# Optimization experiments

Measured on AMD Instinct MI355X. Metric: run time of the kernel, lower is better.

## Reference

```python
import jax, jax.numpy as jnp
import numpy as np

NUM_LAYERS = 3
N = 4096
DIM = 512
TOPK = 8
BIG = 1.0e9
EPS_COS = 1e-8
EPS_NORM = 1e-12
BN_EPS = 1e-5
LAM_K = 64.0
LAM_Z = 16.0
SIGMA_INTRA = 0.99
ALPHA = np.linspace(1.0, 1.2, NUM_LAYERS)
BETA = np.linspace(0.0, 0.0, NUM_LAYERS)


def setup_inputs() -> dict:
    key = jax.random.key(0)
    ks = jax.random.split(key, 6)
    feats = jax.random.normal(ks[0], (NUM_LAYERS, N, DIM), dtype=jnp.float32)
    labels = jax.random.randint(ks[1], (N,), 0, 64, dtype=jnp.int64)
    fc1_w = jax.random.normal(ks[2], (NUM_LAYERS, DIM, DIM), dtype=jnp.float32) * (1.0 / np.sqrt(DIM))
    fc2_w = jax.random.normal(ks[3], (NUM_LAYERS, DIM, DIM), dtype=jnp.float32) * (1.0 / np.sqrt(DIM))
    bn_gamma = jnp.ones((NUM_LAYERS, DIM), dtype=jnp.float32)
    bn_beta = jnp.zeros((NUM_LAYERS, DIM), dtype=jnp.float32)
    proj_w = jax.random.normal(ks[4], (768, DIM), dtype=jnp.float32) * (1.0 / np.sqrt(DIM))
    return {"feats": feats, "labels": labels, "fc1_w": fc1_w, "fc2_w": fc2_w,
            "bn_gamma": bn_gamma, "bn_beta": bn_beta, "proj_w": proj_w}


def _l2norm(x, axis=-1):
    return x / jnp.maximum(jnp.linalg.norm(x, axis=axis, keepdims=True), EPS_NORM)


def _pairwise_cosine(G):
    Gn = _l2norm(G)
    sim = Gn @ Gn.T
    return jnp.clip(sim, -1.0 + EPS_COS, 1.0 - EPS_COS)


def _knn_mask(sim, base_mask, topk):
    n = sim.shape[0]
    masked = (sim - BIG * jnp.eye(n, dtype=sim.dtype)) * base_mask - (1.0 - base_mask) * BIG
    k = min(topk, max(n - 1, 1))
    idx = jax.lax.top_k(masked, k)[1]  # [N, k]
    st = jnp.zeros_like(sim).at[jnp.arange(n)[:, None], idx].set(1.0)
    return jnp.maximum(st, st.T)


def _build_intra_inter(sim, labels, topk):
    same = (labels[None, :] == labels[:, None]).astype(sim.dtype)
    diff = 1.0 - same
    m_intra = _knn_mask(sim, same, topk)
    m_inter = _knn_mask(sim, diff, topk)
    sim_intra = jnp.maximum(sim * m_intra, 0.0)
    sim_inter = jnp.maximum(sim * m_inter, 0.0)
    return sim_intra, sim_inter


def _normalize_sym(sim_graph, eps=1e-8):
    d = jnp.maximum(sim_graph.sum(axis=1), eps)
    dinv = d ** -0.5
    return dinv[:, None] * sim_graph * dinv[None, :]  # == diag(dinv) @ S @ diag(dinv)


def _diffusion(K, t_diff=1):
    out = K
    for _ in range(max(t_diff - 1, 0)):
        out = out @ K
    return out


def _bn_train(x, gamma, beta):
    m = x.mean(axis=0)
    v = x.var(axis=0)  # biased, as torch BN training
    return (x - m) / jnp.sqrt(v + BN_EPS) * gamma + beta


def _gam(S, G, w1, w2, gamma, beta):
    Z = S @ (G @ w1.T)
    Z = jax.nn.relu(_bn_train(Z, gamma, beta))
    Z = S @ (Z @ w2.T)
    return Z + G


def reference(feats, labels, fc1_w, fc2_w, bn_gamma, bn_beta, proj_w):
    n = feats.shape[1]
    eye = jnp.eye(n, dtype=feats.dtype)
    same = (labels[None, :] == labels[:, None]).astype(feats.dtype)

    K_list, Z_list = [], []
    for i in range(NUM_LAYERS):
        G = feats[i]
        sim = _pairwise_cosine(G)
        sim_intra, sim_inter = _build_intra_inter(sim, labels, TOPK)
        sim_graph = float(ALPHA[i]) * sim_intra + float(BETA[i]) * sim_inter + 1e-6 * eye
        S = _normalize_sym(sim_graph)
        K = _diffusion(S, t_diff=1)
        Z = _gam(S, G, fc1_w[i], fc2_w[i], bn_gamma[i], bn_beta[i])
        K_list.append(K)
        Z_list.append(Z)

    loss_K = jnp.zeros((), dtype=feats.dtype)
    loss_Z = jnp.zeros((), dtype=feats.dtype)
    for i in range(1, NUM_LAYERS):
        K_tgt = jax.lax.stop_gradient(K_list[i])
        loss_K = loss_K + jnp.mean((K_list[i - 1] - K_tgt) ** 2)
        Zp = _l2norm(Z_list[i - 1] @ proj_w.T)
        Zc = _l2norm(Z_list[i] @ proj_w.T)
        loss_Z = loss_Z + jnp.mean((Zp - jax.lax.stop_gradient(Zc)) ** 2)

    K_idea = _diffusion(same * SIGMA_INTRA, t_diff=1)
    loss_idea = jnp.mean((K_list[-1] - K_idea) ** 2)
    return LAM_K * loss_K + LAM_Z * loss_Z + loss_idea
```

## Files before the change

### kernel.cpp

```cpp
#include <hip/hip_runtime.h>
#include <math.h>

#define NROWS 4096
#define DIM   512
#define NCLS  64
#define CAP   128
#define PD    768
#define NL    3

typedef __attribute__((ext_vector_type(8))) short short8v;
typedef __attribute__((ext_vector_type(4))) float f32x4;

__device__ __forceinline__ unsigned short f2bf(float f) {
  unsigned u = __float_as_uint(f);
  unsigned r = (u + 0x7FFF + ((u >> 16) & 1)) >> 16;
  return (unsigned short)r;
}

__device__ __forceinline__ float waveReduce(float v) {
#pragma unroll
  for (int o = 32; o > 0; o >>= 1) v += __shfl_down(v, o);
  return v;
}

__device__ __forceinline__ float blockReduce(float v) {
  __shared__ float sh[4];
  int lane = threadIdx.x & 63, wv = threadIdx.x >> 6;
  v = waveReduce(v);
  if (lane == 0) sh[wv] = v;
  __syncthreads();
  float t = 0.f;
  if (threadIdx.x == 0) {
    int nw = (blockDim.x + 63) >> 6;
    for (int i = 0; i < nw; ++i) t += sh[i];
  }
  return t;
}

__global__ void k_zerof(float* p, int n) {
  for (int i = blockIdx.x * blockDim.x + threadIdx.x; i < n; i += gridDim.x * blockDim.x) p[i] = 0.f;
}

__global__ __launch_bounds__(256) void k_hist(const int* __restrict__ labels, int* __restrict__ chunkCnt) {
  __shared__ int h[NCLS];
  int t = threadIdx.x;
  if (t < NCLS) h[t] = 0;
  __syncthreads();
  atomicAdd(&h[labels[blockIdx.x * 256 + t]], 1);
  __syncthreads();
  if (t < NCLS) chunkCnt[blockIdx.x * NCLS + t] = h[t];
}

__global__ void k_scan(const int* __restrict__ chunkCnt, int* __restrict__ cnt,
                       int* __restrict__ off, int* __restrict__ chunkBase) {
  __shared__ int sc[NCLS];
  int c = threadIdx.x;
  int tot = 0;
  for (int b = 0; b < 16; ++b) tot += chunkCnt[b * NCLS + c];
  cnt[c] = tot;
  sc[c] = tot;
  __syncthreads();
  if (c == 0) {
    int s = 0;
    for (int i = 0; i < NCLS; ++i) { int tv = sc[i]; sc[i] = s; s += tv; }
  }
  __syncthreads();
  int run = sc[c];
  off[c] = run;
  for (int b = 0; b < 16; ++b) { chunkBase[b * NCLS + c] = run; run += chunkCnt[b * NCLS + c]; }
  if (c == 0) off[NCLS] = NROWS;
}

__global__ __launch_bounds__(256) void k_scatter(const int* __restrict__ labels, const int* __restrict__ chunkBase,
                                                 int* __restrict__ perm, int* __restrict__ clsp) {
  __shared__ int lab[256];
  int t = threadIdx.x;
  int r = blockIdx.x * 256 + t;
  int c = labels[r];
  lab[t] = c;
  __syncthreads();
  int rank = 0;
  for (int j = 0; j < t; ++j) rank += (lab[j] == c);
  int pos = chunkBase[blockIdx.x * NCLS + c] + rank;
  perm[pos] = r;
  clsp[pos] = c;
}

__global__ __launch_bounds__(128) void k_prep(const float* __restrict__ feats, const int* __restrict__ perm,
                                              unsigned short* __restrict__ Gpb, float* __restrict__ invn) {
  __shared__ float red[2];
  int l = blockIdx.y;
  const float* G = feats + (size_t)l * NROWS * DIM;
  unsigned short* Gp = Gpb + (size_t)l * NROWS * DIM;
  int row = blockIdx.x, t = threadIdx.x;
  const float4* src = (const float4*)(G + (size_t)perm[row] * DIM);
  float4 v = src[t];
  ushort4 b;
  b.x = f2bf(v.x); b.y = f2bf(v.y); b.z = f2bf(v.z); b.w = f2bf(v.w);
  *(ushort4*)(Gp + (size_t)row * DIM + t * 4) = b;
  float ss = v.x * v.x + v.y * v.y + v.z * v.z + v.w * v.w;
  ss = waveReduce(ss);
  if ((t & 63) == 0) red[t >> 6] = ss;
  __syncthreads();
  if (t == 0) invn[l * NROWS + row] = 1.f / fmaxf(sqrtf(red[0] + red[1]), 1e-12f);
}

__global__ void k_tobf16(const float4* __restrict__ src, ushort4* __restrict__ dst, int n4) {
  int i = blockIdx.x * blockDim.x + threadIdx.x;
  if (i < n4) {
    float4 v = src[i];
    ushort4 o;
    o.x = f2bf(v.x); o.y = f2bf(v.y); o.z = f2bf(v.z); o.w = f2bf(v.w);
    dst[i] = o;
  }
}

__global__ __launch_bounds__(256) void k_sim(const unsigned short* __restrict__ Gpb,
                                             const float* __restrict__ invn,
                                             const int* __restrict__ cnt, const int* __restrict__ off,
                                             float* __restrict__ sim) {
  int l = blockIdx.z;
  const unsigned short* Gp = Gpb + (size_t)l * NROWS * DIM;
  const float* inv = invn + (size_t)l * NROWS;
  float* sm = sim + (size_t)l * NCLS * CAP * CAP;
  int c = blockIdx.y;
  int n = min(cnt[c], CAP);
  int ti = blockIdx.x >> 2, tj = blockIdx.x & 3;
  if (ti * 32 >= n || tj * 32 >= n) return;
  int base = off[c];
  __shared__ short As[32][40];
  __shared__ short Bs[32][40];
  const int t = threadIdx.x;
  const int lane = t & 63, wv = t >> 6;
  const int qi = wv >> 1, qj = wv & 1;
  const int fr = lane & 15, kg = lane >> 4;
  const int half = t >> 7, tt = t & 127;
  const int srow = tt >> 2, scol = (tt & 3) * 8;
  int gr = (half ? tj : ti) * 32 + srow;
  const unsigned short* ps = Gp + (size_t)(base + min(gr, n - 1)) * DIM + scol;
  short* dst = half ? &Bs[srow][scol] : &As[srow][scol];
  f32x4 acc = {};
  for (int k0 = 0; k0 < DIM; k0 += 32) {
    short8v v = *(const short8v*)(ps + k0);
    __syncthreads();
    *(short8v*)dst = v;
    __syncthreads();
    short8v af = *(const short8v*)&As[qi * 16 + fr][kg * 8];
    short8v bf = *(const short8v*)&Bs[qj * 16 + fr][kg * 8];
    acc = __builtin_amdgcn_mfma_f32_16x16x32_bf16(af, bf, acc, 0, 0, 0);
  }
  int gj = tj * 32 + qj * 16 + fr;
  int r0 = ti * 32 + qi * 16 + kg * 4;
  if (gj < n) {
    float sj = inv[base + gj];
#pragma unroll
    for (int r = 0; r < 4; ++r) {
      int gi = r0 + r;
      if (gi < n) {
        float v = acc[r] * inv[base + gi] * sj;
        v = fminf(fmaxf(v, -1.0f + 1e-8f), 1.0f - 1e-8f);
        sm[((size_t)c * CAP + gi) * CAP + gj] = v;
      }
    }
  }
}

__global__ __launch_bounds__(64) void k_topk(const float* __restrict__ sim, const int* __restrict__ cnt,
                                             const int* __restrict__ off, const int* __restrict__ clsp,
                                             int* __restrict__ t8) {
  int l = blockIdx.y;
  const float* sm = sim + (size_t)l * NCLS * CAP * CAP;
  int* t8l = t8 + (size_t)l * NROWS * 8;
  int pr = blockIdx.x * 64 + threadIdx.x;
  if (pr >= NROWS) return;
  int c = clsp[pr];
  int n = min(cnt[c], CAP);
  int loc = pr - off[c];
  const float* row = sm + ((size_t)c * CAP + loc) * CAP;
  float bv[8]; int bi[8];
#pragma unroll
  for (int q = 0; q < 8; ++q) { bv[q] = -3e38f; bi[q] = -1; }
  for (int j = 0; j < n; ++j) {
    if (j == loc) continue;
    float v = row[j];
    if (v > bv[7]) {
      bv[7] = v; bi[7] = j;
#pragma unroll
      for (int q = 7; q > 0; --q) {
        if (bv[q] > bv[q - 1]) {
          float tv = bv[q]; bv[q] = bv[q - 1]; bv[q - 1] = tv;
          int tq = bi[q]; bi[q] = bi[q - 1]; bi[q - 1] = tq;
        }
      }
    }
  }
#pragma unroll
  for (int q = 0; q < 8; ++q) t8l[pr * 8 + q] = bi[q];
}

__global__ __launch_bounds__(256) void k_buildS1(const float* __restrict__ sim, const int* __restrict__ cnt,
                                                 const int* __restrict__ off, const int* __restrict__ t8,
                                                 float* __restrict__ S, float* __restrict__ dinv) {
  int l = blockIdx.z;
  float alpha = 1.0f + 0.1f * l;
  const float* sm = sim + (size_t)l * NCLS * CAP * CAP;
  float* Sl = S + (size_t)l * NCLS * CAP * CAP;
  const int* t8l = t8 + (size_t)l * NROWS * 8;
  float* dv = dinv + (size_t)l * NCLS * CAP;
  int c = blockIdx.x;
  int n = min(cnt[c], CAP);
  int i0 = blockIdx.y * 32;
  if (i0 >= n) return;
  int base = off[c];
  __shared__ int sh8[CAP * 8];
  for (int i = threadIdx.x; i < n * 8; i += 256) sh8[i] = t8l[base * 8 + i];
  __syncthreads();
  int r = threadIdx.x >> 3;
  int lj = threadIdx.x & 7;
  int i = i0 + r;
  float d = 0.f;
  if (i < n) {
    int my8[8];
#pragma unroll
    for (int q = 0; q < 8; ++q) my8[q] = sh8[i * 8 + q];
    const float* srow = sm + ((size_t)c * CAP + i) * CAP;
    float* wrow = Sl + ((size_t)c * CAP + i) * CAP;
    for (int j = lj; j < n; j += 8) {
      float w;
      if (j == i) w = 1e-6f;
      else {
        bool m = false;
#pragma unroll
        for (int q = 0; q < 8; ++q) m = m || (my8[q] == j) || (sh8[j * 8 + q] == i);
        w = m ? alpha * fmaxf(srow[j], 0.f) : 0.f;
      }
      wrow[j] = w;
      d += w;
    }
  }
  d += __shfl_xor(d, 1);
  d += __shfl_xor(d, 2);
  d += __shfl_xor(d, 4);
  if (lj == 0 && i < n) dv[c * CAP + i] = 1.f / sqrtf(fmaxf(d, 1e-8f));
}

__global__ __launch_bounds__(256) void k_buildS2(float* __restrict__ S, const float* __restrict__ dinv,
                                                 const int* __restrict__ cnt) {
  int l = blockIdx.z;
  float* Sl = S + (size_t)l * NCLS * CAP * CAP;
  const float* dv = dinv + (size_t)l * NCLS * CAP;
  int c = blockIdx.x;
  int n = min(cnt[c], CAP);
  int i0 = blockIdx.y * 32;
  if (i0 >= n) return;
  __shared__ float sd[CAP];
  for (int k = threadIdx.x; k < n; k += 256) sd[k] = dv[c * CAP + k];
  __syncthreads();
  for (int p = threadIdx.x; p < 32 * CAP; p += 256) {
    int r = p >> 7, j = p & (CAP - 1);
    int i = i0 + r;
    if (i < n && j < n)
      Sl[((size_t)c * CAP + i) * CAP + j] *= sd[i] * sd[j];
  }
}

__global__ __launch_bounds__(256) void k_gemm_bf16(const short* __restrict__ A, const short* __restrict__ B,
                                                   float* __restrict__ C, int N,
                                                   long sA, long sB, long sC) {
  int l = blockIdx.z;
  A += (size_t)l * sA; B += (size_t)l * sB; C += (size_t)l * sC;
  __shared__ short As[128][40];
  __shared__ short Bs[64][40];
  const int row0 = blockIdx.x * 128, col0 = blockIdx.y * 64;
  const int t = threadIdx.x;
  const int lane = t & 63, wv = t >> 6;
  const int fr = lane & 15, kg = lane >> 4;
  const int sra = t >> 1, ska = (t & 1) * 16;
  const int srb = t >> 2, skb = (t & 3) * 8;
  const short* pa = A + (size_t)(row0 + sra) * DIM + ska;
  const short* pb = B + (size_t)(col0 + srb) * DIM + skb;
  f32x4 acc[2][4] = {};
  for (int kt = 0; kt < DIM; kt += 32) {
    short8v a0 = *(const short8v*)(pa + kt);
    short8v a1 = *(const short8v*)(pa + kt + 8);
    short8v b0 = *(const short8v*)(pb + kt);
    __syncthreads();
    *(short8v*)&As[sra][ska] = a0;
    *(short8v*)&As[sra][ska + 8] = a1;
    *(short8v*)&Bs[srb][skb] = b0;
    __syncthreads();
    short8v af[2], bf[4];
#pragma unroll
    for (int i = 0; i < 2; ++i) af[i] = *(const short8v*)&As[wv * 32 + i * 16 + fr][kg * 8];
#pragma unroll
    for (int j = 0; j < 4; ++j) bf[j] = *(const short8v*)&Bs[j * 16 + fr][kg * 8];
#pragma unroll
    for (int i = 0; i < 2; ++i)
#pragma unroll
      for (int j = 0; j < 4; ++j)
        acc[i][j] = __builtin_amdgcn_mfma_f32_16x16x32_bf16(af[i], bf[j], acc[i][j], 0, 0, 0);
  }
#pragma unroll
  for (int i = 0; i < 2; ++i) {
    int r0 = row0 + wv * 32 + i * 16 + kg * 4;
#pragma unroll
    for (int j = 0; j < 4; ++j) {
      int cc = col0 + j * 16 + fr;
#pragma unroll
      for (int r = 0; r < 4; ++r)
        C[(size_t)(r0 + r) * N + cc] = acc[i][j][r];
    }
  }
}

__global__ __launch_bounds__(256) void k_spmm4(const float* __restrict__ S, const float* __restrict__ X,
                                               const float* __restrict__ Gfeat, const int* __restrict__ perm,
                                               float* __restrict__ Y, unsigned short* __restrict__ Yb,
                                               const int* __restrict__ cnt, const int* __restrict__ off) {
  int l = blockIdx.z >> 2;
  int zc = blockIdx.z & 3;
  const float* Sl = S + (size_t)l * NCLS * CAP * CAP;
  const float4* X4 = (const float4*)(X + (size_t)l * NROWS * DIM);
  const float4* G4 = Gfeat ? (const float4*)(Gfeat + (size_t)l * NROWS * DIM) : (const float4*)nullptr;
  float4* Y4 = Y ? (float4*)(Y + (size_t)l * NROWS * DIM) : (float4*)nullptr;
  ushort4* Yb4 = Yb ? (ushort4*)(Yb + (size_t)l * NROWS * DIM) : (ushort4*)nullptr;
  int c = blockIdx.x;
  int n = min(cnt[c], CAP);
  int i0 = zc * 32;
  if (i0 >= n) return;
  int base = off[c];
  int col4 = blockIdx.y * 64 + (threadIdx.x & 63);
  int ty = threadIdx.x >> 6;
  __shared__ float sS[32][CAP];
  for (int idx = threadIdx.x; idx < 32 * n; idx += 256) {
    int r = idx / n, j = idx - r * n;
    sS[r][j] = (i0 + r < n) ? Sl[((size_t)c * CAP + i0 + r) * CAP + j] : 0.f;
  }
  __syncthreads();
  float4 acc[8];
#pragma unroll
  for (int ii = 0; ii < 8; ++ii) acc[ii] = make_float4(0.f, 0.f, 0.f, 0.f);
  for (int j = 0; j < n; ++j) {
    float4 x = X4[(size_t)(base + j) * 128 + col4];
#pragma unroll
    for (int ii = 0; ii < 8; ++ii) {
      float s = sS[ty * 8 + ii][j];
      acc[ii].x += s * x.x;
      acc[ii].y += s * x.y;
      acc[ii].z += s * x.z;
      acc[ii].w += s * x.w;
    }
  }
#pragma unroll
  for (int ii = 0; ii < 8; ++ii) {
    int r = i0 + ty * 8 + ii;
    if (r < n) {
      size_t o = (size_t)(base + r) * 128 + col4;
      float4 v = acc[ii];
      if (G4) {
        float4 g = G4[(size_t)perm[base + r] * 128 + col4];
        v.x += g.x; v.y += g.y; v.z += g.z; v.w += g.w;
      }
      if (Yb4) {
        ushort4 ob;
        ob.x = f2bf(v.x); ob.y = f2bf(v.y); ob.z = f2bf(v.z); ob.w = f2bf(v.w);
        Yb4[o] = ob;
      } else {
        Y4[o] = v;
      }
    }
  }
}

#define PARTSZ (size_t)((NROWS / 32) * 1024)

__global__ __launch_bounds__(256) void k_colstats(const float* __restrict__ X, float* __restrict__ part) {
  int l = blockIdx.y;
  const float* Xl = X + (size_t)l * NROWS * DIM;
  float* pl = part + (size_t)l * PARTSZ;
  int rb = blockIdx.x, t = threadIdx.x;
#pragma unroll
  for (int cp = 0; cp < 2; ++cp) {
    int col = cp * 256 + t;
    float s = 0.f, s2 = 0.f;
    for (int r = 0; r < 32; ++r) {
      float v = Xl[(size_t)(rb * 32 + r) * DIM + col];
      s += v; s2 += v * v;
    }
    pl[rb * 1024 + col] = s;
    pl[rb * 1024 + 512 + col] = s2;
  }
}

__global__ __launch_bounds__(64) void k_bnfin(const float* __restrict__ part, const float* __restrict__ gamma,
                                              const float* __restrict__ beta, float* __restrict__ sc) {
  int l = blockIdx.y;
  const float* pl = part + (size_t)l * PARTSZ;
  int k = blockIdx.x * 64 + threadIdx.x;
  float s = 0.f, s2 = 0.f;
  for (int b = 0; b < NROWS / 32; ++b) {
    s += pl[b * 1024 + k];
    s2 += pl[b * 1024 + 512 + k];
  }
  float m = s * (1.f / NROWS);
  float var = s2 * (1.f / NROWS) - m * m;
  float sg = gamma[l * DIM + k] / sqrtf(var + 1e-5f);
  sc[l * 2 * DIM + k] = sg;
  sc[l * 2 * DIM + DIM + k] = beta[l * DIM + k] - m * sg;
}

__global__ __launch_bounds__(256) void k_bnrelu(const float4* __restrict__ X, const float* __restrict__ sc,
                                                ushort4* __restrict__ Yb) {
  int l = blockIdx.y;
  const float4* Xl = X + (size_t)l * (NROWS * DIM / 4);
  const float* scl = sc + (size_t)l * 2 * DIM;
  ushort4* Yl = Yb + (size_t)l * (NROWS * DIM / 4);
  int i = blockIdx.x * blockDim.x + threadIdx.x;
  int cb = (i * 4) & (DIM - 1);
  float4 v = Xl[i];
  ushort4 o;
  o.x = f2bf(fmaxf(v.x * scl[cb + 0] + scl[DIM + cb + 0], 0.f));
  o.y = f2bf(fmaxf(v.y * scl[cb + 1] + scl[DIM + cb + 1], 0.f));
  o.z = f2bf(fmaxf(v.z * scl[cb + 2] + scl[DIM + cb + 2], 0.f));
  o.w = f2bf(fmaxf(v.w * scl[cb + 3] + scl[DIM + cb + 3], 0.f));
  Yl[i] = o;
}

__global__ __launch_bounds__(192) void k_rownormP(float* __restrict__ P) {
  __shared__ float red[3];
  __shared__ float s_inv;
  int l = blockIdx.y;
  float* Pl = P + (size_t)l * NROWS * PD;
  int row = blockIdx.x, t = threadIdx.x;
  float4* p = (float4*)(Pl + (size_t)row * PD);
  float4 v = p[t];
  float ss = v.x * v.x + v.y * v.y + v.z * v.z + v.w * v.w;
  ss = waveReduce(ss);
  if ((t & 63) == 0) red[t >> 6] = ss;
  __syncthreads();
  if (t == 0) s_inv = 1.f / fmaxf(sqrtf(red[0] + red[1] + red[2]), 1e-12f);
  __syncthreads();
  float inv = s_inv;
  v.x *= inv; v.y *= inv; v.z *= inv; v.w *= inv;
  p[t] = v;
}

__global__ __launch_bounds__(256) void k_lossdiff(const float* __restrict__ P, int n, float coef,
                                                  float* __restrict__ acc) {
  int y = blockIdx.y;
  const float* A = P + (size_t)y * NROWS * PD;
  const float* B = A + (size_t)NROWS * PD;
  float s = 0.f;
  for (int i = blockIdx.x * blockDim.x + threadIdx.x; i < n; i += gridDim.x * blockDim.x) {
    float d = A[i] - B[i];
    s += d * d;
  }
  s = blockReduce(s);
  if (threadIdx.x == 0) atomicAdd(acc, s * coef);
}

__global__ __launch_bounds__(256) void k_lossS(const float* __restrict__ S, const int* __restrict__ cnt,
                                               float target, float cK, float cI,
                                               float* __restrict__ acc) {
  int y = blockIdx.y;
  const float* Sa = S + (size_t)y * NCLS * CAP * CAP;
  const float* Sb = nullptr;
  float coef;
  if (y < 2) { Sb = Sa + (size_t)NCLS * CAP * CAP; coef = cK; }
  else { Sa = S + (size_t)2 * NCLS * CAP * CAP; coef = cI; }
  int c = blockIdx.x;
  int n = min(cnt[c], CAP);
  float s = 0.f;
  for (int p = threadIdx.x; p < CAP * CAP; p += 256) {
    int i = p >> 7, j = p & (CAP - 1);
    if (i < n && j < n) {
      size_t o = ((size_t)c * CAP + i) * CAP + j;
      float d = Sb ? (Sa[o] - Sb[o]) : (Sa[o] - target);
      s += d * d;
    }
  }
  s = blockReduce(s);
  if (threadIdx.x == 0) atomicAdd(acc, s * coef);
}

__global__ void k_final(const float* __restrict__ acc, float* __restrict__ out) {
  if (threadIdx.x == 0) out[0] = acc[0];
}

extern "C" void kernel_launch(void* const* d_in, const int* in_sizes, int n_in,
                              void* d_out, int out_size, void* d_ws, size_t ws_size,
                              hipStream_t stream) {
  const float* feats = (const float*)d_in[0];
  const int* labels = (const int*)d_in[1];
  const float* fc1 = (const float*)d_in[2];
  const float* fc2 = (const float*)d_in[3];
  const float* gamma = (const float*)d_in[4];
  const float* beta = (const float*)d_in[5];
  const float* proj = (const float*)d_in[6];
  float* out = (float*)d_out;

  char* w = (char*)d_ws;
  auto alloc = [&](size_t bytes) { char* p = w; w += (bytes + 255) & ~(size_t)255; return p; };
  float* bufA = (float*)alloc((size_t)NL * NROWS * DIM * 4);
  float* bufB = (float*)alloc((size_t)NL * NROWS * DIM * 4);
  unsigned short* Gpb = (unsigned short*)alloc((size_t)NL * NROWS * DIM * 2);
  unsigned short* actb = (unsigned short*)alloc((size_t)NL * NROWS * DIM * 2);
  unsigned short* W1b = (unsigned short*)alloc((size_t)NL * DIM * DIM * 2);
  unsigned short* W2b = (unsigned short*)alloc((size_t)NL * DIM * DIM * 2);
  unsigned short* Pjb = (unsigned short*)alloc((size_t)PD * DIM * 2);
  float* sim  = (float*)alloc((size_t)NL * NCLS * CAP * CAP * 4);
  float* S    = (float*)alloc((size_t)NL * NCLS * CAP * CAP * 4);
  float* P    = (float*)alloc((size_t)NL * NROWS * PD * 4);
  float* invn = (float*)alloc((size_t)NL * NROWS * 4);
  float* dinv = (float*)alloc((size_t)NL * NCLS * CAP * 4);
  float* part = (float*)alloc((size_t)NL * PARTSZ * 4);
  float* bnsc = (float*)alloc((size_t)NL * 2 * DIM * 4);
  float* acc  = (float*)alloc(256);
  int* cnt  = (int*)alloc(NCLS * 4);
  int* offc = (int*)alloc((NCLS + 1) * 4);
  int* perm = (int*)alloc(NROWS * 4);
  int* clsp = (int*)alloc(NROWS * 4);
  int* t8   = (int*)alloc((size_t)NL * NROWS * 8 * 4);
  int* chunkCnt  = (int*)alloc(16 * NCLS * 4);
  int* chunkBase = (int*)alloc(16 * NCLS * 4);

  const float LAM_K = 64.f, LAM_Z = 16.f, SIGMA = 0.99f;
  const float cK = LAM_K / ((float)NROWS * (float)NROWS);
  const float cZ = LAM_Z / ((float)NROWS * (float)PD);
  const float cI = 1.f / ((float)NROWS * (float)NROWS);
  const long sAct = (long)NROWS * DIM;
  const long sW = (long)DIM * DIM;

  hipLaunchKernelGGL(k_zerof, dim3(1), dim3(64), 0, stream, acc, 4);
  hipLaunchKernelGGL(k_hist, dim3(16), dim3(256), 0, stream, labels, chunkCnt);
  hipLaunchKernelGGL(k_scan, dim3(1), dim3(64), 0, stream, chunkCnt, cnt, offc, chunkBase);
  hipLaunchKernelGGL(k_scatter, dim3(16), dim3(256), 0, stream, labels, chunkBase, perm, clsp);
  hipLaunchKernelGGL(k_tobf16, dim3((NL * DIM * DIM / 4 + 255) / 256), dim3(256), 0, stream,
                     (const float4*)fc1, (ushort4*)W1b, NL * DIM * DIM / 4);
  hipLaunchKernelGGL(k_tobf16, dim3((NL * DIM * DIM / 4 + 255) / 256), dim3(256), 0, stream,
                     (const float4*)fc2, (ushort4*)W2b, NL * DIM * DIM / 4);
  hipLaunchKernelGGL(k_tobf16, dim3((PD * DIM / 4 + 255) / 256), dim3(256), 0, stream,
                     (const float4*)proj, (ushort4*)Pjb, PD * DIM / 4);

  hipLaunchKernelGGL(k_prep, dim3(NROWS, NL), dim3(128), 0, stream, feats, perm, Gpb, invn);
  hipLaunchKernelGGL(k_sim, dim3(16, NCLS, NL), dim3(256), 0, stream, Gpb, invn, cnt, offc, sim);
  hipLaunchKernelGGL(k_topk, dim3(NROWS / 64, NL), dim3(64), 0, stream, sim, cnt, offc, clsp, t8);
  hipLaunchKernelGGL(k_buildS1, dim3(NCLS, CAP / 32, NL), dim3(256), 0, stream, sim, cnt, offc, t8, S, dinv);
  hipLaunchKernelGGL(k_buildS2, dim3(NCLS, CAP / 32, NL), dim3(256), 0, stream, S, dinv, cnt);

  hipLaunchKernelGGL(k_gemm_bf16, dim3(NROWS / 128, DIM / 64, NL), dim3(256), 0, stream,
                     (const short*)Gpb, (const short*)W1b, bufA, DIM, sAct, sW, (long)NROWS * DIM);
  hipLaunchKernelGGL(k_spmm4, dim3(NCLS, DIM / 256, 4 * NL), dim3(256), 0, stream, S, bufA,
                     (const float*)nullptr, (const int*)nullptr, bufB, (unsigned short*)nullptr, cnt, offc);
  hipLaunchKernelGGL(k_colstats, dim3(NROWS / 32, NL), dim3(256), 0, stream, bufB, part);
  hipLaunchKernelGGL(k_bnfin, dim3(DIM / 64, NL), dim3(64), 0, stream, part, gamma, beta, bnsc);
  hipLaunchKernelGGL(k_bnrelu, dim3(NROWS * DIM / 4 / 256, NL), dim3(256), 0, stream,
                     (const float4*)bufB, bnsc, (ushort4*)actb);
  hipLaunchKernelGGL(k_gemm_bf16, dim3(NROWS / 128, DIM / 64, NL), dim3(256), 0, stream,
                     (const short*)actb, (const short*)W2b, bufB, DIM, sAct, sW, (long)NROWS * DIM);
  hipLaunchKernelGGL(k_spmm4, dim3(NCLS, DIM / 256, 4 * NL), dim3(256), 0, stream, S, bufB,
                     feats, perm, (float*)nullptr, actb, cnt, offc);
  hipLaunchKernelGGL(k_gemm_bf16, dim3(NROWS / 128, PD / 64, NL), dim3(256), 0, stream,
                     (const short*)actb, (const short*)Pjb, P, PD, sAct, 0L, (long)NROWS * PD);
  hipLaunchKernelGGL(k_rownormP, dim3(NROWS, NL), dim3(192), 0, stream, P);

  hipLaunchKernelGGL(k_lossS, dim3(NCLS, 3), dim3(256), 0, stream, S, cnt, SIGMA, cK, cI, acc);
  hipLaunchKernelGGL(k_lossdiff, dim3(512, 2), dim3(256), 0, stream, P, NROWS * PD, cZ, acc);

  hipLaunchKernelGGL(k_final, dim3(1), dim3(64), 0, stream, acc, out);
}
```

Measured before the change: 278.1 us.

## Enlarge GEMM tile to 128x128 with direct global-to-LDS loads; merge small launches

The bf16 GEMM moves from 128x64 to 128x128 output tiles, with a 2x2 wave layout where each wave computes 64x64. Tiles are now loaded with global_load_lds, which writes straight to LDS instead of going through registers, and the LDS padding is dropped. The three weight-conversion launches become one kernel, and zeroing the accumulator moves into k_scan, removing several tiny launches. The larger tile improves reuse per load but halves the grid and raises register pressure, and the unpadded LDS layout may cause bank conflicts on the fragment reads.

```diff
diff --git a/kernel.cpp b/kernel.cpp
--- a/kernel.cpp
+++ b/kernel.cpp
@@ -1,5 +1,6 @@
 #include <hip/hip_runtime.h>
 #include <math.h>
+#include <stdint.h>
 
 #define NROWS 4096
 #define DIM   512
@@ -17,6 +18,14 @@
   return (unsigned short)r;
 }
 
+__device__ __forceinline__ void gload_lds16(const void* g, void* l) {
+  auto* lp = reinterpret_cast<__attribute__((address_space(3))) unsigned int*>(
+      reinterpret_cast<uintptr_t>(l));
+  const auto* gp = reinterpret_cast<const __attribute__((address_space(1))) unsigned int*>(
+      reinterpret_cast<uintptr_t>(g));
+  __builtin_amdgcn_global_load_lds(gp, lp, 16, 0, 0);
+}
+
 __device__ __forceinline__ float waveReduce(float v) {
 #pragma unroll
   for (int o = 32; o > 0; o >>= 1) v += __shfl_down(v, o);
@@ -37,10 +46,6 @@
   return t;
 }
 
-__global__ void k_zerof(float* p, int n) {
-  for (int i = blockIdx.x * blockDim.x + threadIdx.x; i < n; i += gridDim.x * blockDim.x) p[i] = 0.f;
-}
-
 __global__ __launch_bounds__(256) void k_hist(const int* __restrict__ labels, int* __restrict__ chunkCnt) {
   __shared__ int h[NCLS];
   int t = threadIdx.x;
@@ -52,9 +57,10 @@
 }
 
 __global__ void k_scan(const int* __restrict__ chunkCnt, int* __restrict__ cnt,
-                       int* __restrict__ off, int* __restrict__ chunkBase) {
+                       int* __restrict__ off, int* __restrict__ chunkBase, float* __restrict__ acc) {
   __shared__ int sc[NCLS];
   int c = threadIdx.x;
+  if (c < 8) acc[c] = 0.f;
   int tot = 0;
   for (int b = 0; b < 16; ++b) tot += chunkCnt[b * NCLS + c];
   cnt[c] = tot;
@@ -105,14 +111,22 @@
   if (t == 0) invn[l * NROWS + row] = 1.f / fmaxf(sqrtf(red[0] + red[1]), 1e-12f);
 }
 
-__global__ void k_tobf16(const float4* __restrict__ src, ushort4* __restrict__ dst, int n4) {
-  int i = blockIdx.x * blockDim.x + threadIdx.x;
-  if (i < n4) {
-    float4 v = src[i];
-    ushort4 o;
-    o.x = f2bf(v.x); o.y = f2bf(v.y); o.z = f2bf(v.z); o.w = f2bf(v.w);
-    dst[i] = o;
-  }
+__global__ __launch_bounds__(256) void k_tobf16all(const float4* __restrict__ fc1, const float4* __restrict__ fc2,
+                                                   const float4* __restrict__ proj,
+                                                   ushort4* __restrict__ w1, ushort4* __restrict__ w2,
+                                                   ushort4* __restrict__ pj) {
+  const int nW = NL * DIM * DIM / 4;
+  const int nP = PD * DIM / 4;
+  int i = blockIdx.x * 256 + threadIdx.x;
+  const float4* src; ushort4* dst; int k;
+  if (i < nW) { src = fc1; dst = w1; k = i; }
+  else if (i < 2 * nW) { src = fc2; dst = w2; k = i - nW; }
+  else if (i < 2 * nW + nP) { src = proj; dst = pj; k = i - 2 * nW; }
+  else return;
+  float4 v = src[k];
+  ushort4 o;
+  o.x = f2bf(v.x); o.y = f2bf(v.y); o.z = f2bf(v.z); o.w = f2bf(v.w);
+  dst[k] = o;
 }
 
 __global__ __launch_bounds__(256) void k_sim(const unsigned short* __restrict__ Gpb,
@@ -269,43 +283,42 @@
                                                    long sA, long sB, long sC) {
   int l = blockIdx.z;
   A += (size_t)l * sA; B += (size_t)l * sB; C += (size_t)l * sC;
-  __shared__ short As[128][40];
-  __shared__ short Bs[64][40];
-  const int row0 = blockIdx.x * 128, col0 = blockIdx.y * 64;
+  __shared__ __align__(16) short As[128][32];
+  __shared__ __align__(16) short Bs[128][32];
+  const int row0 = blockIdx.x * 128, col0 = blockIdx.y * 128;
   const int t = threadIdx.x;
   const int lane = t & 63, wv = t >> 6;
+  const int wm = wv >> 1, wn = wv & 1;
   const int fr = lane & 15, kg = lane >> 4;
-  const int sra = t >> 1, ska = (t & 1) * 16;
-  const int srb = t >> 2, skb = (t & 3) * 8;
-  const short* pa = A + (size_t)(row0 + sra) * DIM + ska;
-  const short* pb = B + (size_t)(col0 + srb) * DIM + skb;
-  f32x4 acc[2][4] = {};
+  const int srow = lane >> 2, skb = (lane & 3) * 8;
+  const short* pa = A + (size_t)(row0 + wv * 32 + srow) * DIM + skb;
+  const short* pb = B + (size_t)(col0 + wv * 32 + srow) * DIM + skb;
+  f32x4 acc[4][4] = {};
   for (int kt = 0; kt < DIM; kt += 32) {
-    short8v a0 = *(const short8v*)(pa + kt);
-    short8v a1 = *(const short8v*)(pa + kt + 8);
-    short8v b0 = *(const short8v*)(pb + kt);
     __syncthreads();
-    *(short8v*)&As[sra][ska] = a0;
-    *(short8v*)&As[sra][ska + 8] = a1;
-    *(short8v*)&Bs[srb][skb] = b0;
+    gload_lds16(pa + kt, &As[wv * 32][0]);
+    gload_lds16(pa + kt + (size_t)16 * DIM, &As[wv * 32 + 16][0]);
+    gload_lds16(pb + kt, &Bs[wv * 32][0]);
+    gload_lds16(pb + kt + (size_t)16 * DIM, &Bs[wv * 32 + 16][0]);
     __syncthreads();
-    short8v af[2], bf[4];
-#pragma unroll
-    for (int i = 0; i < 2; ++i) af[i] = *(const short8v*)&As[wv * 32 + i * 16 + fr][kg * 8];
-#pragma unroll
-    for (int j = 0; j < 4; ++j) bf[j] = *(const short8v*)&Bs[j * 16 + fr][kg * 8];
-#pragma unroll
-    for (int i = 0; i < 2; ++i)
+    short8v af[4], bf[4];
+#pragma unroll
+    for (int i = 0; i < 4; ++i) {
+      af[i] = *(const short8v*)&As[wm * 64 + i * 16 + fr][kg * 8];
+      bf[i] = *(const short8v*)&Bs[wn * 64 + i * 16 + fr][kg * 8];
+    }
+#pragma unroll
+    for (int i = 0; i < 4; ++i)
 #pragma unroll
       for (int j = 0; j < 4; ++j)
         acc[i][j] = __builtin_amdgcn_mfma_f32_16x16x32_bf16(af[i], bf[j], acc[i][j], 0, 0, 0);
   }
 #pragma unroll
-  for (int i = 0; i < 2; ++i) {
-    int r0 = row0 + wv * 32 + i * 16 + kg * 4;
+  for (int i = 0; i < 4; ++i) {
+    int r0 = row0 + wm * 64 + i * 16 + kg * 4;
 #pragma unroll
     for (int j = 0; j < 4; ++j) {
-      int cc = col0 + j * 16 + fr;
+      int cc = col0 + wn * 64 + j * 16 + fr;
 #pragma unroll
       for (int r = 0; r < 4; ++r)
         C[(size_t)(r0 + r) * N + cc] = acc[i][j][r];
@@ -531,16 +544,12 @@
   const long sAct = (long)NROWS * DIM;
   const long sW = (long)DIM * DIM;
 
-  hipLaunchKernelGGL(k_zerof, dim3(1), dim3(64), 0, stream, acc, 4);
   hipLaunchKernelGGL(k_hist, dim3(16), dim3(256), 0, stream, labels, chunkCnt);
-  hipLaunchKernelGGL(k_scan, dim3(1), dim3(64), 0, stream, chunkCnt, cnt, offc, chunkBase);
+  hipLaunchKernelGGL(k_scan, dim3(1), dim3(64), 0, stream, chunkCnt, cnt, offc, chunkBase, acc);
   hipLaunchKernelGGL(k_scatter, dim3(16), dim3(256), 0, stream, labels, chunkBase, perm, clsp);
-  hipLaunchKernelGGL(k_tobf16, dim3((NL * DIM * DIM / 4 + 255) / 256), dim3(256), 0, stream,
-                     (const float4*)fc1, (ushort4*)W1b, NL * DIM * DIM / 4);
-  hipLaunchKernelGGL(k_tobf16, dim3((NL * DIM * DIM / 4 + 255) / 256), dim3(256), 0, stream,
-                     (const float4*)fc2, (ushort4*)W2b, NL * DIM * DIM / 4);
-  hipLaunchKernelGGL(k_tobf16, dim3((PD * DIM / 4 + 255) / 256), dim3(256), 0, stream,
-                     (const float4*)proj, (ushort4*)Pjb, PD * DIM / 4);
+  hipLaunchKernelGGL(k_tobf16all, dim3((2 * NL * DIM * DIM / 4 + PD * DIM / 4 + 255) / 256), dim3(256), 0, stream,
+                     (const float4*)fc1, (const float4*)fc2, (const float4*)proj,
+                     (ushort4*)W1b, (ushort4*)W2b, (ushort4*)Pjb);
 
   hipLaunchKernelGGL(k_prep, dim3(NROWS, NL), dim3(128), 0, stream, feats, perm, Gpb, invn);
   hipLaunchKernelGGL(k_sim, dim3(16, NCLS, NL), dim3(256), 0, stream, Gpb, invn, cnt, offc, sim);
@@ -548,7 +557,7 @@
   hipLaunchKernelGGL(k_buildS1, dim3(NCLS, CAP / 32, NL), dim3(256), 0, stream, sim, cnt, offc, t8, S, dinv);
   hipLaunchKernelGGL(k_buildS2, dim3(NCLS, CAP / 32, NL), dim3(256), 0, stream, S, dinv, cnt);
 
-  hipLaunchKernelGGL(k_gemm_bf16, dim3(NROWS / 128, DIM / 64, NL), dim3(256), 0, stream,
+  hipLaunchKernelGGL(k_gemm_bf16, dim3(NROWS / 128, DIM / 128, NL), dim3(256), 0, stream,
                      (const short*)Gpb, (const short*)W1b, bufA, DIM, sAct, sW, (long)NROWS * DIM);
   hipLaunchKernelGGL(k_spmm4, dim3(NCLS, DIM / 256, 4 * NL), dim3(256), 0, stream, S, bufA,
                      (const float*)nullptr, (const int*)nullptr, bufB, (unsigned short*)nullptr, cnt, offc);
@@ -556,11 +565,11 @@
   hipLaunchKernelGGL(k_bnfin, dim3(DIM / 64, NL), dim3(64), 0, stream, part, gamma, beta, bnsc);
   hipLaunchKernelGGL(k_bnrelu, dim3(NROWS * DIM / 4 / 256, NL), dim3(256), 0, stream,
                      (const float4*)bufB, bnsc, (ushort4*)actb);
-  hipLaunchKernelGGL(k_gemm_bf16, dim3(NROWS / 128, DIM / 64, NL), dim3(256), 0, stream,
+  hipLaunchKernelGGL(k_gemm_bf16, dim3(NROWS / 128, DIM / 128, NL), dim3(256), 0, stream,
                      (const short*)actb, (const short*)W2b, bufB, DIM, sAct, sW, (long)NROWS * DIM);
   hipLaunchKernelGGL(k_spmm4, dim3(NCLS, DIM / 256, 4 * NL), dim3(256), 0, stream, S, bufB,
                      feats, perm, (float*)nullptr, actb, cnt, offc);
-  hipLaunchKernelGGL(k_gemm_bf16, dim3(NROWS / 128, PD / 64, NL), dim3(256), 0, stream,
+  hipLaunchKernelGGL(k_gemm_bf16, dim3(NROWS / 128, PD / 128, NL), dim3(256), 0, stream,
                      (const short*)actb, (const short*)Pjb, P, PD, sAct, 0L, (long)NROWS * PD);
   hipLaunchKernelGGL(k_rownormP, dim3(NROWS, NL), dim3(192), 0, stream, P);
 
```

After: 281.6 us. About the same (+1.3%).
